# Kernel tuning notes

Hardware: AMD Instinct MI355X
Metric: run time of the kernel (lower is better)

Reference implementation:

```python
import jax, jax.numpy as jnp
import numpy as np

N_NODES = 200000
N_EDGES = 6400000
NUM_GRAPHS = 20000
D_NODE, D_EDGE, D_MSG = 5, 4, 10


def setup_inputs() -> dict:
    key = jax.random.key(0)
    ks = jax.random.split(key, 16)
    inp = {
        "edge_index": jax.random.randint(ks[0], (2, N_EDGES), 0, N_NODES, dtype=jnp.int64)
                      if jax.config.jax_enable_x64 else
                      jax.random.randint(ks[0], (2, N_EDGES), 0, N_NODES, dtype=jnp.int32),
        "node_attr": jax.random.normal(ks[1], (N_NODES, D_NODE), dtype=jnp.float32),
        "edge_attr": jax.random.normal(ks[2], (N_EDGES, D_EDGE), dtype=jnp.float32),
        "batch": jnp.sort(jax.random.randint(ks[3], (N_NODES,), 0, NUM_GRAPHS, dtype=jnp.int32)),
        "num_graphs": NUM_GRAPHS,
        # MPL_1: Linear(2*D_NODE + D_EDGE -> 10)
        "w_mpl": jax.random.normal(ks[4], (2 * D_NODE + D_EDGE, D_MSG), dtype=jnp.float32) * 0.3,
        "b_mpl": jnp.zeros((D_MSG,), dtype=jnp.float32),
        "w1": jax.random.normal(ks[5], (10, 10), dtype=jnp.float32) * 0.3,
        "b1": jnp.zeros((10,), dtype=jnp.float32),
        "w2": jax.random.normal(ks[6], (10, 5), dtype=jnp.float32) * 0.3,
        "b2": jnp.zeros((5,), dtype=jnp.float32),
        "w3": jax.random.normal(ks[7], (5, 5), dtype=jnp.float32) * 0.3,
        "b3": jnp.zeros((5,), dtype=jnp.float32),
        "w4": jax.random.normal(ks[8], (5, 1), dtype=jnp.float32) * 0.3,
        "b4": jnp.zeros((1,), dtype=jnp.float32),
    }
    return inp


def reference(edge_index, node_attr, edge_attr, batch, num_graphs,
              w_mpl, b_mpl, w1, b1, w2, b2, w3, b3, w4, b4):
    src, dst = edge_index[0], edge_index[1]
    n_nodes = node_attr.shape[0]
    # MPL_1: gather endpoints, concat with edge features, MLP, scatter-sum to dst
    edge_in = jnp.concatenate(
        [node_attr[src], node_attr[dst], edge_attr], axis=-1)  # [E, 14]
    msg = jax.nn.relu(edge_in @ w_mpl + b_mpl)                 # [E, 10]
    x = jax.ops.segment_sum(msg, dst, num_segments=n_nodes)    # [N, 10]
    # node MLP head
    x = jax.nn.relu(x @ w1 + b1)
    x = jax.nn.relu(x @ w2 + b2)
    # segment_coo(reduce='sum') over sorted batch index -> per-graph pooling
    x = jax.ops.segment_sum(x, batch, num_segments=num_graphs,
                            indices_are_sorted=True)           # [G, 5]
    x = jax.nn.relu(x @ w3 + b3)
    return x @ w4 + b4                                         # [G, 1]
```

## Files before the change

kernel.cpp:

```cpp
#include <hip/hip_runtime.h>

#define DN 5
#define DE 4
#define DM 10
#define NB_SCAT 512
#define BKT_SH 8
#define BKT_NODES 256
#define MAXBKT 1024

__global__ __launch_bounds__(256) void pack_kernel(
    const float* __restrict__ node_attr, float4* __restrict__ napack, int N)
{
    int n = blockIdx.x * 256 + threadIdx.x;
    if (n >= N) return;
    const float* r = node_attr + (size_t)n * DN;
    napack[2 * (size_t)n]     = make_float4(r[0], r[1], r[2], r[3]);
    napack[2 * (size_t)n + 1] = make_float4(r[4], 0.f, 0.f, 0.f);
}

__global__ __launch_bounds__(256) void hist_kernel(
    const int* __restrict__ ei, unsigned* __restrict__ cnt,
    int E, int chunk, int nbk)
{
    __shared__ unsigned hist[MAXBKT];
    int t = threadIdx.x, b = blockIdx.x;
    for (int j = t; j < nbk; j += 256) hist[j] = 0;
    __syncthreads();

    int e0 = b * chunk, e1 = min(E, e0 + chunk);
    for (int i = e0 + t; i < e1; i += 256) {
        int d = ei[(size_t)E + i];
        atomicAdd(&hist[d >> BKT_SH], 1u);
    }
    __syncthreads();
    for (int j = t; j < nbk; j += 256)
        cnt[(size_t)j * NB_SCAT + b] = hist[j];
}

__global__ __launch_bounds__(256) void scan1_kernel(
    unsigned* __restrict__ cnt, unsigned* __restrict__ bsum, int len)
{
    __shared__ unsigned lds[256];
    int t = threadIdx.x;
    int i = blockIdx.x * 256 + t;
    unsigned v = (i < len) ? cnt[i] : 0u;
    lds[t] = v; __syncthreads();
#pragma unroll
    for (int o = 1; o < 256; o <<= 1) {
        unsigned add = (t >= o) ? lds[t - o] : 0u;
        __syncthreads();
        lds[t] += add;
        __syncthreads();
    }
    unsigned incl = lds[t];
    if (i < len) cnt[i] = incl - v;
    if (t == 255) bsum[blockIdx.x] = incl;
}

__global__ __launch_bounds__(1024) void scan2_kernel(unsigned* __restrict__ bsum, int nsb)
{
    __shared__ unsigned lds[1024];
    int t = threadIdx.x;
    int base = t * 4;
    unsigned v0 = (base + 0 < nsb) ? bsum[base + 0] : 0u;
    unsigned v1 = (base + 1 < nsb) ? bsum[base + 1] : 0u;
    unsigned v2 = (base + 2 < nsb) ? bsum[base + 2] : 0u;
    unsigned v3 = (base + 3 < nsb) ? bsum[base + 3] : 0u;
    unsigned tot = v0 + v1 + v2 + v3;
    lds[t] = tot; __syncthreads();
#pragma unroll
    for (int o = 1; o < 1024; o <<= 1) {
        unsigned add = (t >= o) ? lds[t - o] : 0u;
        __syncthreads();
        lds[t] += add;
        __syncthreads();
    }
    unsigned run = lds[t] - tot;
    if (base + 0 < nsb) bsum[base + 0] = run; run += v0;
    if (base + 1 < nsb) bsum[base + 1] = run; run += v1;
    if (base + 2 < nsb) bsum[base + 2] = run; run += v2;
    if (base + 3 < nsb) bsum[base + 3] = run;
}

__global__ __launch_bounds__(256) void scan3_kernel(
    unsigned* __restrict__ cnt, const unsigned* __restrict__ bsum, int len)
{
    int i = blockIdx.x * 256 + threadIdx.x;
    if (i < len) cnt[i] += bsum[i >> 8];
}

__global__ __launch_bounds__(256) void scatter_kernel(
    const int* __restrict__ ei, const float* __restrict__ edge_attr,
    const unsigned* __restrict__ cnt,
    unsigned* __restrict__ rec_meta, float4* __restrict__ rec_ea,
    int E, int chunk, int nbk)
{
    __shared__ unsigned woff[MAXBKT];
    int t = threadIdx.x, b = blockIdx.x;
    for (int j = t; j < nbk; j += 256) woff[j] = cnt[(size_t)j * NB_SCAT + b];
    __syncthreads();

    int e0 = b * chunk, e1 = min(E, e0 + chunk);
    for (int i = e0 + t; i < e1; i += 256) {
        int s = ei[i];
        int d = ei[(size_t)E + i];
        float4 ea = reinterpret_cast<const float4*>(edge_attr)[i];
        unsigned p = atomicAdd(&woff[d >> BKT_SH], 1u);
        rec_meta[p] = (unsigned)s | ((unsigned)(d & 255) << 18);
        rec_ea[p] = ea;
    }
}

__global__ __launch_bounds__(256) void gather_kernel(
    const unsigned* __restrict__ rec_meta, const float4* __restrict__ rec_ea,
    const unsigned* __restrict__ cnt,
    const float4* __restrict__ napack,
    const float* __restrict__ w_mpl, const float* __restrict__ b_mpl,
    float* __restrict__ xpart, size_t xstride,
    int E, int N, int nbk, int nsplit)
{
    __shared__ float acc[BKT_NODES * DM];
    __shared__ float pdl[BKT_NODES * 12];
    __shared__ float sws[50];
    __shared__ float swe[40];

    int t = threadIdx.x;
    int j  = blockIdx.x / nsplit;
    int sp = blockIdx.x - j * nsplit;
    int nb0 = j * BKT_NODES;

    if (t < 50)       sws[t] = w_mpl[t];
    else if (t < 90)  swe[t - 50] = w_mpl[100 + (t - 50)];

    for (int i = t; i < BKT_NODES * DM; i += 256) acc[i] = 0.f;

    {
        int n = nb0 + t;
        float a0 = 0.f, a1 = 0.f, a2 = 0.f, a3 = 0.f, a4 = 0.f;
        if (n < N) {
            float4 r0 = napack[2 * (size_t)n];
            float4 r1 = napack[2 * (size_t)n + 1];
            a0 = r0.x; a1 = r0.y; a2 = r0.z; a3 = r0.w; a4 = r1.x;
        }
#pragma unroll
        for (int q = 0; q < DM; ++q) {
            float v = b_mpl[q];
            v = fmaf(a0, w_mpl[50 + q],      v);
            v = fmaf(a1, w_mpl[60 + q],      v);
            v = fmaf(a2, w_mpl[70 + q],      v);
            v = fmaf(a3, w_mpl[80 + q],      v);
            v = fmaf(a4, w_mpl[90 + q],      v);
            pdl[t * 12 + q] = v;
        }
    }
    __syncthreads();

    unsigned start = cnt[(size_t)j * NB_SCAT];
    unsigned end   = (j + 1 < nbk) ? cnt[(size_t)(j + 1) * NB_SCAT] : (unsigned)E;
    unsigned blen  = end - start;
    unsigned csz   = (blen + nsplit - 1) / nsplit;
    unsigned ss    = start + (unsigned)sp * csz;
    unsigned se    = min(end, ss + csz);

    for (unsigned i0 = ss + t; i0 < se; i0 += 4u * 256u) {
        unsigned meta[4]; float4 ea[4]; bool act[4];
#pragma unroll
        for (int u = 0; u < 4; ++u) {
            unsigned i = i0 + (unsigned)u * 256u;
            act[u] = (i < se);
            if (act[u]) { meta[u] = rec_meta[i]; ea[u] = rec_ea[i]; }
        }
        float4 n0[4], n1[4];
#pragma unroll
        for (int u = 0; u < 4; ++u)
            if (act[u]) {
                size_t s = meta[u] & 0x3FFFFu;
                n0[u] = napack[2 * s];
                n1[u] = napack[2 * s + 1];
            }
#pragma unroll
        for (int u = 0; u < 4; ++u) {
            if (!act[u]) continue;
            int dl = meta[u] >> 18;
            const float* pr = &pdl[dl * 12];
            float4 p0 = *reinterpret_cast<const float4*>(pr);
            float4 p1 = *reinterpret_cast<const float4*>(pr + 4);
            float2 p2 = *reinterpret_cast<const float2*>(pr + 8);
            float m[DM] = {p0.x, p0.y, p0.z, p0.w, p1.x, p1.y, p1.z, p1.w, p2.x, p2.y};
            float a0 = n0[u].x, a1 = n0[u].y, a2 = n0[u].z, a3 = n0[u].w, a4 = n1[u].x;
            float4 e4 = ea[u];
#pragma unroll
            for (int q = 0; q < DM; ++q) {
                float v = m[q];
                v = fmaf(a0, sws[q],        v);
                v = fmaf(a1, sws[10 + q],   v);
                v = fmaf(a2, sws[20 + q],   v);
                v = fmaf(a3, sws[30 + q],   v);
                v = fmaf(a4, sws[40 + q],   v);
                v = fmaf(e4.x, swe[q],      v);
                v = fmaf(e4.y, swe[10 + q], v);
                v = fmaf(e4.z, swe[20 + q], v);
                v = fmaf(e4.w, swe[30 + q], v);
                if (v > 0.f) atomicAdd(&acc[dl * DM + q], v);
            }
        }
    }
    __syncthreads();

    float* dst = xpart + (size_t)sp * xstride + (size_t)nb0 * DM;
    for (int i = t; i < BKT_NODES * DM; i += 256) dst[i] = acc[i];
}

__global__ __launch_bounds__(256) void combine_kernel(
    const float* __restrict__ xpart, size_t xstride,
    const int* __restrict__ batch,
    const float* __restrict__ w1, const float* __restrict__ b1,
    const float* __restrict__ w2, const float* __restrict__ b2,
    float* __restrict__ gacc, int N, int nsplit)
{
    __shared__ float s1[100], sb1[10], s2[50], sb2[5];
    int t = threadIdx.x;
    if (t < 100)      s1[t] = w1[t];
    else if (t < 110) sb1[t - 100] = b1[t - 100];
    else if (t < 160) s2[t - 110] = w2[t - 110];
    else if (t < 165) sb2[t - 160] = b2[t - 160];
    __syncthreads();

    int n = blockIdx.x * blockDim.x + t;
    bool valid = (n < N);
    int g = 0x7fffffff;
    float h2[5] = {0.f, 0.f, 0.f, 0.f, 0.f};

    if (valid) {
        float x[DM];
#pragma unroll
        for (int q = 0; q < DM; ++q) x[q] = 0.f;
        for (int sp = 0; sp < nsplit; ++sp) {
            const float2* row = reinterpret_cast<const float2*>(
                xpart + (size_t)sp * xstride + (size_t)n * DM);
#pragma unroll
            for (int h = 0; h < 5; ++h) {
                float2 v = row[h];
                x[2 * h] += v.x; x[2 * h + 1] += v.y;
            }
        }

        float h1[10];
#pragma unroll
        for (int q = 0; q < 10; ++q) h1[q] = sb1[q];
#pragma unroll
        for (int k = 0; k < 10; ++k)
#pragma unroll
            for (int q = 0; q < 10; ++q) h1[q] = fmaf(x[k], s1[k * 10 + q], h1[q]);
#pragma unroll
        for (int q = 0; q < 10; ++q) h1[q] = fmaxf(h1[q], 0.f);
#pragma unroll
        for (int q = 0; q < 5; ++q) h2[q] = sb2[q];
#pragma unroll
        for (int k = 0; k < 10; ++k)
#pragma unroll
            for (int q = 0; q < 5; ++q) h2[q] = fmaf(h1[k], s2[k * 5 + q], h2[q]);
#pragma unroll
        for (int q = 0; q < 5; ++q) h2[q] = fmaxf(h2[q], 0.f);
        g = batch[n];
    }

    int lane = t & 63;
#pragma unroll
    for (int o = 1; o < 64; o <<= 1) {
        int go = __shfl_down(g, o);
        float v0 = __shfl_down(h2[0], o);
        float v1 = __shfl_down(h2[1], o);
        float v2 = __shfl_down(h2[2], o);
        float v3 = __shfl_down(h2[3], o);
        float v4 = __shfl_down(h2[4], o);
        if (lane + o < 64 && go == g) {
            h2[0] += v0; h2[1] += v1; h2[2] += v2; h2[3] += v3; h2[4] += v4;
        }
    }
    int gp = __shfl_up(g, 1);
    bool head = (lane == 0) || (gp != g);
    if (head && g != 0x7fffffff) {
#pragma unroll
        for (int q = 0; q < 5; ++q)
            if (h2[q] != 0.f) unsafeAtomicAdd(&gacc[(size_t)g * 5 + q], h2[q]);
    }
}

__global__ __launch_bounds__(256) void graph_head_kernel(
    const float* __restrict__ gacc,
    const float* __restrict__ w3, const float* __restrict__ b3,
    const float* __restrict__ w4, const float* __restrict__ b4,
    float* __restrict__ out, int G)
{
    __shared__ float s3[25], sb3[5], s4[5], sb4[1];
    int t = threadIdx.x;
    if (t < 25)       s3[t] = w3[t];
    else if (t < 30)  sb3[t - 25] = b3[t - 25];
    else if (t < 35)  s4[t - 30] = w4[t - 30];
    else if (t == 35) sb4[0] = b4[0];
    __syncthreads();

    int g = blockIdx.x * blockDim.x + t;
    if (g >= G) return;

    float x[5];
#pragma unroll
    for (int k = 0; k < 5; ++k) x[k] = gacc[(size_t)g * 5 + k];

    float o = sb4[0];
#pragma unroll
    for (int q = 0; q < 5; ++q) {
        float h = sb3[q];
#pragma unroll
        for (int k = 0; k < 5; ++k) h = fmaf(x[k], s3[k * 5 + q], h);
        h = fmaxf(h, 0.f);
        o = fmaf(h, s4[q], o);
    }
    out[g] = o;
}

extern "C" void kernel_launch(void* const* d_in, const int* in_sizes, int n_in,
                              void* d_out, int out_size, void* d_ws, size_t ws_size,
                              hipStream_t stream)
{
    const int*   ei        = (const int*)d_in[0];
    const float* node_attr = (const float*)d_in[1];
    const float* edge_attr = (const float*)d_in[2];
    const int*   batch     = (const int*)d_in[3];
    const float* w_mpl = (const float*)d_in[5];
    const float* b_mpl = (const float*)d_in[6];
    const float* w1    = (const float*)d_in[7];
    const float* b1    = (const float*)d_in[8];
    const float* w2    = (const float*)d_in[9];
    const float* b2    = (const float*)d_in[10];
    const float* w3    = (const float*)d_in[11];
    const float* b3    = (const float*)d_in[12];
    const float* w4    = (const float*)d_in[13];
    const float* b4    = (const float*)d_in[14];
    float* out = (float*)d_out;

    const int E = in_sizes[0] / 2;
    const int N = in_sizes[1] / DN;
    const int G = out_size;

    const int nbk   = (N + BKT_NODES - 1) / BKT_NODES;
    const int chunk = (E + NB_SCAT - 1) / NB_SCAT;
    const int len   = nbk * NB_SCAT;
    const int nsb   = (len + 255) / 256;

    char* p = (char*)d_ws;
    float4*   rec_ea   = (float4*)p;   p += (size_t)E * 16;
    float4*   napack   = (float4*)p;   p += (size_t)N * 32;
    unsigned* rec_meta = (unsigned*)p; p += (size_t)E * 4;
    unsigned* cnt      = (unsigned*)p; p += (size_t)len * 4;
    unsigned* bsum     = (unsigned*)p; p += (size_t)((nsb + 3) & ~3) * 4;
    float*    gacc     = (float*)p;    p += (size_t)G * 5 * 4;
    float*    xpart    = (float*)p;

    size_t used = (size_t)(p - (char*)d_ws);
    size_t xstride = (size_t)nbk * BKT_NODES * DM;
    int nsplit = 8;
    while (nsplit > 1 && used + (size_t)nsplit * xstride * 4 > ws_size) nsplit >>= 1;

    hipMemsetAsync(gacc, 0, (size_t)G * 5 * 4, stream);

    pack_kernel<<<(N + 255) / 256, 256, 0, stream>>>(node_attr, napack, N);
    hist_kernel<<<NB_SCAT, 256, 0, stream>>>(ei, cnt, E, chunk, nbk);
    scan1_kernel<<<nsb, 256, 0, stream>>>(cnt, bsum, len);
    scan2_kernel<<<1, 1024, 0, stream>>>(bsum, nsb);
    scan3_kernel<<<nsb, 256, 0, stream>>>(cnt, bsum, len);
    scatter_kernel<<<NB_SCAT, 256, 0, stream>>>(ei, edge_attr, cnt, rec_meta, rec_ea, E, chunk, nbk);
    gather_kernel<<<nbk * nsplit, 256, 0, stream>>>(rec_meta, rec_ea, cnt, napack,
                                                    w_mpl, b_mpl, xpart, xstride, E, N, nbk, nsplit);
    combine_kernel<<<nbk, 256, 0, stream>>>(xpart, xstride, batch, w1, b1, w2, b2, gacc, N, nsplit);
    graph_head_kernel<<<(G + 255) / 256, 256, 0, stream>>>(gacc, w3, b3, w4, b4, out, G);
}
```

Before: 621.7 us.

## Fuse pack into histogram, row-wise scan, and interleave edge records

Folds the node-attribute packing into the histogram kernel and raises the number of scatter and histogram blocks from 512 to 2048. The three-pass global scan is replaced by a per-bucket row scan plus a single small base scan. Scatter now batches four edges per thread and writes each edge as one 32-byte record combining meta and edge attributes, instead of separate meta and attribute arrays. The cnt buffer now aliases the xpart region. This cuts kernel launches and improves load concurrency, but each record grows from 20 to 32 bytes, which adds write and read traffic in scatter and gather.

```diff
diff --git a/kernel.cpp b/kernel.cpp
--- a/kernel.cpp
+++ b/kernel.cpp
@@ -3,27 +3,26 @@
 #define DN 5
 #define DE 4
 #define DM 10
-#define NB_SCAT 512
+#define NB 2048
 #define BKT_SH 8
 #define BKT_NODES 256
 #define MAXBKT 1024
 
-__global__ __launch_bounds__(256) void pack_kernel(
-    const float* __restrict__ node_attr, float4* __restrict__ napack, int N)
-{
-    int n = blockIdx.x * 256 + threadIdx.x;
-    if (n >= N) return;
-    const float* r = node_attr + (size_t)n * DN;
-    napack[2 * (size_t)n]     = make_float4(r[0], r[1], r[2], r[3]);
-    napack[2 * (size_t)n + 1] = make_float4(r[4], 0.f, 0.f, 0.f);
-}
-
-__global__ __launch_bounds__(256) void hist_kernel(
-    const int* __restrict__ ei, unsigned* __restrict__ cnt,
-    int E, int chunk, int nbk)
+__global__ __launch_bounds__(256) void hist_pack_kernel(
+    const int* __restrict__ ei, const float* __restrict__ node_attr,
+    float4* __restrict__ napack, unsigned* __restrict__ cnt,
+    int E, int chunk, int nbk, int N)
 {
     __shared__ unsigned hist[MAXBKT];
     int t = threadIdx.x, b = blockIdx.x;
+
+    int n = b * 256 + t;
+    if (n < N) {
+        const float* r = node_attr + (size_t)n * DN;
+        napack[2 * (size_t)n]     = make_float4(r[0], r[1], r[2], r[3]);
+        napack[2 * (size_t)n + 1] = make_float4(r[4], 0.f, 0.f, 0.f);
+    }
+
     for (int j = t; j < nbk; j += 256) hist[j] = 0;
     __syncthreads();
 
@@ -34,17 +33,20 @@
     }
     __syncthreads();
     for (int j = t; j < nbk; j += 256)
-        cnt[(size_t)j * NB_SCAT + b] = hist[j];
-}
-
-__global__ __launch_bounds__(256) void scan1_kernel(
-    unsigned* __restrict__ cnt, unsigned* __restrict__ bsum, int len)
+        cnt[(size_t)j * NB + b] = hist[j];
+}
+
+__global__ __launch_bounds__(256) void scan_rows_kernel(
+    unsigned* __restrict__ cnt, unsigned* __restrict__ rowtotal)
 {
     __shared__ unsigned lds[256];
-    int t = threadIdx.x;
-    int i = blockIdx.x * 256 + t;
-    unsigned v = (i < len) ? cnt[i] : 0u;
-    lds[t] = v; __syncthreads();
+    int j = blockIdx.x, t = threadIdx.x;
+    unsigned* row = cnt + (size_t)j * NB;
+
+    unsigned v[8], s = 0;
+#pragma unroll
+    for (int u = 0; u < 8; ++u) { v[u] = row[t * 8 + u]; s += v[u]; }
+    lds[t] = s; __syncthreads();
 #pragma unroll
     for (int o = 1; o < 256; o <<= 1) {
         unsigned add = (t >= o) ? lds[t - o] : 0u;
@@ -52,22 +54,20 @@
         lds[t] += add;
         __syncthreads();
     }
-    unsigned incl = lds[t];
-    if (i < len) cnt[i] = incl - v;
-    if (t == 255) bsum[blockIdx.x] = incl;
-}
-
-__global__ __launch_bounds__(1024) void scan2_kernel(unsigned* __restrict__ bsum, int nsb)
+    unsigned excl = lds[t] - s;
+#pragma unroll
+    for (int u = 0; u < 8; ++u) { row[t * 8 + u] = excl; excl += v[u]; }
+    if (t == 255) rowtotal[j] = lds[255];
+}
+
+__global__ __launch_bounds__(1024) void scan_base_kernel(
+    const unsigned* __restrict__ rowtotal, unsigned* __restrict__ gbase,
+    int nbk, int E)
 {
     __shared__ unsigned lds[1024];
     int t = threadIdx.x;
-    int base = t * 4;
-    unsigned v0 = (base + 0 < nsb) ? bsum[base + 0] : 0u;
-    unsigned v1 = (base + 1 < nsb) ? bsum[base + 1] : 0u;
-    unsigned v2 = (base + 2 < nsb) ? bsum[base + 2] : 0u;
-    unsigned v3 = (base + 3 < nsb) ? bsum[base + 3] : 0u;
-    unsigned tot = v0 + v1 + v2 + v3;
-    lds[t] = tot; __syncthreads();
+    unsigned v = (t < nbk) ? rowtotal[t] : 0u;
+    lds[t] = v; __syncthreads();
 #pragma unroll
     for (int o = 1; o < 1024; o <<= 1) {
         unsigned add = (t >= o) ? lds[t - o] : 0u;
@@ -75,45 +75,48 @@
         lds[t] += add;
         __syncthreads();
     }
-    unsigned run = lds[t] - tot;
-    if (base + 0 < nsb) bsum[base + 0] = run; run += v0;
-    if (base + 1 < nsb) bsum[base + 1] = run; run += v1;
-    if (base + 2 < nsb) bsum[base + 2] = run; run += v2;
-    if (base + 3 < nsb) bsum[base + 3] = run;
-}
-
-__global__ __launch_bounds__(256) void scan3_kernel(
-    unsigned* __restrict__ cnt, const unsigned* __restrict__ bsum, int len)
-{
-    int i = blockIdx.x * 256 + threadIdx.x;
-    if (i < len) cnt[i] += bsum[i >> 8];
+    unsigned excl = lds[t] - v;
+    if (t < nbk)       gbase[t] = excl;
+    else if (t == nbk) gbase[t] = (unsigned)E;
 }
 
 __global__ __launch_bounds__(256) void scatter_kernel(
     const int* __restrict__ ei, const float* __restrict__ edge_attr,
-    const unsigned* __restrict__ cnt,
-    unsigned* __restrict__ rec_meta, float4* __restrict__ rec_ea,
-    int E, int chunk, int nbk)
+    const unsigned* __restrict__ cnt, const unsigned* __restrict__ gbase,
+    float4* __restrict__ rec4, int E, int chunk, int nbk)
 {
     __shared__ unsigned woff[MAXBKT];
     int t = threadIdx.x, b = blockIdx.x;
-    for (int j = t; j < nbk; j += 256) woff[j] = cnt[(size_t)j * NB_SCAT + b];
+    for (int j = t; j < nbk; j += 256)
+        woff[j] = gbase[j] + cnt[(size_t)j * NB + b];
     __syncthreads();
 
     int e0 = b * chunk, e1 = min(E, e0 + chunk);
-    for (int i = e0 + t; i < e1; i += 256) {
-        int s = ei[i];
-        int d = ei[(size_t)E + i];
-        float4 ea = reinterpret_cast<const float4*>(edge_attr)[i];
-        unsigned p = atomicAdd(&woff[d >> BKT_SH], 1u);
-        rec_meta[p] = (unsigned)s | ((unsigned)(d & 255) << 18);
-        rec_ea[p] = ea;
+    for (int i0 = e0 + t; i0 < e1; i0 += 4 * 256) {
+        int s[4], d[4]; float4 ea[4]; bool act[4];
+#pragma unroll
+        for (int u = 0; u < 4; ++u) {
+            int i = i0 + u * 256;
+            act[u] = (i < e1);
+            if (act[u]) {
+                s[u] = ei[i];
+                d[u] = ei[(size_t)E + i];
+                ea[u] = reinterpret_cast<const float4*>(edge_attr)[i];
+            }
+        }
+#pragma unroll
+        for (int u = 0; u < 4; ++u) {
+            if (!act[u]) continue;
+            unsigned p = atomicAdd(&woff[d[u] >> BKT_SH], 1u);
+            unsigned meta = (unsigned)s[u] | ((unsigned)(d[u] & 255) << 18);
+            rec4[2 * (size_t)p]     = make_float4(__uint_as_float(meta), ea[u].x, ea[u].y, ea[u].z);
+            rec4[2 * (size_t)p + 1] = make_float4(ea[u].w, 0.f, 0.f, 0.f);
+        }
     }
 }
 
 __global__ __launch_bounds__(256) void gather_kernel(
-    const unsigned* __restrict__ rec_meta, const float4* __restrict__ rec_ea,
-    const unsigned* __restrict__ cnt,
+    const float4* __restrict__ rec4, const unsigned* __restrict__ gbase,
     const float4* __restrict__ napack,
     const float* __restrict__ w_mpl, const float* __restrict__ b_mpl,
     float* __restrict__ xpart, size_t xstride,
@@ -145,62 +148,63 @@
 #pragma unroll
         for (int q = 0; q < DM; ++q) {
             float v = b_mpl[q];
-            v = fmaf(a0, w_mpl[50 + q],      v);
-            v = fmaf(a1, w_mpl[60 + q],      v);
-            v = fmaf(a2, w_mpl[70 + q],      v);
-            v = fmaf(a3, w_mpl[80 + q],      v);
-            v = fmaf(a4, w_mpl[90 + q],      v);
+            v = fmaf(a0, w_mpl[50 + q], v);
+            v = fmaf(a1, w_mpl[60 + q], v);
+            v = fmaf(a2, w_mpl[70 + q], v);
+            v = fmaf(a3, w_mpl[80 + q], v);
+            v = fmaf(a4, w_mpl[90 + q], v);
             pdl[t * 12 + q] = v;
         }
     }
     __syncthreads();
 
-    unsigned start = cnt[(size_t)j * NB_SCAT];
-    unsigned end   = (j + 1 < nbk) ? cnt[(size_t)(j + 1) * NB_SCAT] : (unsigned)E;
+    unsigned start = gbase[j];
+    unsigned end   = gbase[j + 1];
     unsigned blen  = end - start;
     unsigned csz   = (blen + nsplit - 1) / nsplit;
     unsigned ss    = start + (unsigned)sp * csz;
     unsigned se    = min(end, ss + csz);
 
     for (unsigned i0 = ss + t; i0 < se; i0 += 4u * 256u) {
-        unsigned meta[4]; float4 ea[4]; bool act[4];
+        float4 r0[4], r1[4]; bool act[4];
 #pragma unroll
         for (int u = 0; u < 4; ++u) {
             unsigned i = i0 + (unsigned)u * 256u;
             act[u] = (i < se);
-            if (act[u]) { meta[u] = rec_meta[i]; ea[u] = rec_ea[i]; }
+            if (act[u]) { r0[u] = rec4[2 * (size_t)i]; r1[u] = rec4[2 * (size_t)i + 1]; }
         }
         float4 n0[4], n1[4];
 #pragma unroll
         for (int u = 0; u < 4; ++u)
             if (act[u]) {
-                size_t s = meta[u] & 0x3FFFFu;
+                size_t s = __float_as_uint(r0[u].x) & 0x3FFFFu;
                 n0[u] = napack[2 * s];
                 n1[u] = napack[2 * s + 1];
             }
 #pragma unroll
         for (int u = 0; u < 4; ++u) {
             if (!act[u]) continue;
-            int dl = meta[u] >> 18;
+            unsigned meta = __float_as_uint(r0[u].x);
+            int dl = meta >> 18;
             const float* pr = &pdl[dl * 12];
             float4 p0 = *reinterpret_cast<const float4*>(pr);
             float4 p1 = *reinterpret_cast<const float4*>(pr + 4);
             float2 p2 = *reinterpret_cast<const float2*>(pr + 8);
             float m[DM] = {p0.x, p0.y, p0.z, p0.w, p1.x, p1.y, p1.z, p1.w, p2.x, p2.y};
             float a0 = n0[u].x, a1 = n0[u].y, a2 = n0[u].z, a3 = n0[u].w, a4 = n1[u].x;
-            float4 e4 = ea[u];
+            float e0 = r0[u].y, e1 = r0[u].z, e2 = r0[u].w, e3 = r1[u].x;
 #pragma unroll
             for (int q = 0; q < DM; ++q) {
                 float v = m[q];
-                v = fmaf(a0, sws[q],        v);
-                v = fmaf(a1, sws[10 + q],   v);
-                v = fmaf(a2, sws[20 + q],   v);
-                v = fmaf(a3, sws[30 + q],   v);
-                v = fmaf(a4, sws[40 + q],   v);
-                v = fmaf(e4.x, swe[q],      v);
-                v = fmaf(e4.y, swe[10 + q], v);
-                v = fmaf(e4.z, swe[20 + q], v);
-                v = fmaf(e4.w, swe[30 + q], v);
+                v = fmaf(a0, sws[q],      v);
+                v = fmaf(a1, sws[10 + q], v);
+                v = fmaf(a2, sws[20 + q], v);
+                v = fmaf(a3, sws[30 + q], v);
+                v = fmaf(a4, sws[40 + q], v);
+                v = fmaf(e0, swe[q],      v);
+                v = fmaf(e1, swe[10 + q], v);
+                v = fmaf(e2, swe[20 + q], v);
+                v = fmaf(e3, swe[30 + q], v);
                 if (v > 0.f) atomicAdd(&acc[dl * DM + q], v);
             }
         }
@@ -345,34 +349,34 @@
     const int G = out_size;
 
     const int nbk   = (N + BKT_NODES - 1) / BKT_NODES;
-    const int chunk = (E + NB_SCAT - 1) / NB_SCAT;
-    const int len   = nbk * NB_SCAT;
-    const int nsb   = (len + 255) / 256;
+    const int chunk = (E + NB - 1) / NB;
 
     char* p = (char*)d_ws;
-    float4*   rec_ea   = (float4*)p;   p += (size_t)E * 16;
+    float4*   rec4     = (float4*)p;   p += (size_t)E * 32;
     float4*   napack   = (float4*)p;   p += (size_t)N * 32;
-    unsigned* rec_meta = (unsigned*)p; p += (size_t)E * 4;
-    unsigned* cnt      = (unsigned*)p; p += (size_t)len * 4;
-    unsigned* bsum     = (unsigned*)p; p += (size_t)((nsb + 3) & ~3) * 4;
+    unsigned* rowtotal = (unsigned*)p; p += ((size_t)nbk * 4 + 15) & ~15ull;
+    unsigned* gbase    = (unsigned*)p; p += ((size_t)(nbk + 1) * 4 + 15) & ~15ull;
     float*    gacc     = (float*)p;    p += (size_t)G * 5 * 4;
+    unsigned* cnt      = (unsigned*)p;
     float*    xpart    = (float*)p;
-
-    size_t used = (size_t)(p - (char*)d_ws);
+    size_t cnt_bytes = (size_t)nbk * NB * 4;
+
+    size_t used = (size_t)((char*)cnt - (char*)d_ws);
     size_t xstride = (size_t)nbk * BKT_NODES * DM;
     int nsplit = 8;
-    while (nsplit > 1 && used + (size_t)nsplit * xstride * 4 > ws_size) nsplit >>= 1;
+    while (nsplit > 1 &&
+           used + ((cnt_bytes > (size_t)nsplit * xstride * 4) ? cnt_bytes
+                                                              : (size_t)nsplit * xstride * 4) > ws_size)
+        nsplit >>= 1;
 
     hipMemsetAsync(gacc, 0, (size_t)G * 5 * 4, stream);
 
-    pack_kernel<<<(N + 255) / 256, 256, 0, stream>>>(node_attr, napack, N);
-    hist_kernel<<<NB_SCAT, 256, 0, stream>>>(ei, cnt, E, chunk, nbk);
-    scan1_kernel<<<nsb, 256, 0, stream>>>(cnt, bsum, len);
-    scan2_kernel<<<1, 1024, 0, stream>>>(bsum, nsb);
-    scan3_kernel<<<nsb, 256, 0, stream>>>(cnt, bsum, len);
-    scatter_kernel<<<NB_SCAT, 256, 0, stream>>>(ei, edge_attr, cnt, rec_meta, rec_ea, E, chunk, nbk);
-    gather_kernel<<<nbk * nsplit, 256, 0, stream>>>(rec_meta, rec_ea, cnt, napack,
-                                                    w_mpl, b_mpl, xpart, xstride, E, N, nbk, nsplit);
+    hist_pack_kernel<<<NB, 256, 0, stream>>>(ei, node_attr, napack, cnt, E, chunk, nbk, N);
+    scan_rows_kernel<<<nbk, 256, 0, stream>>>(cnt, rowtotal);
+    scan_base_kernel<<<1, 1024, 0, stream>>>(rowtotal, gbase, nbk, E);
+    scatter_kernel<<<NB, 256, 0, stream>>>(ei, edge_attr, cnt, gbase, rec4, E, chunk, nbk);
+    gather_kernel<<<nbk * nsplit, 256, 0, stream>>>(rec4, gbase, napack, w_mpl, b_mpl,
+                                                    xpart, xstride, E, N, nbk, nsplit);
     combine_kernel<<<nbk, 256, 0, stream>>>(xpart, xstride, batch, w1, b1, w2, b2, gacc, N, nsplit);
     graph_head_kernel<<<(G + 255) / 256, 256, 0, stream>>>(gacc, w3, b3, w4, b4, out, G);
 }
```

Result: faster. 585.1 us (-5.9%).
